# Kernel optimization log

Measured on AMD Instinct MI355X. Metric: run time of the kernel, lower is better.

Reference implementation:

```python
import jax, jax.numpy as jnp
import numpy as np

B, T, D_IN = 512, 128, 256
H1, H2 = 1024, 1024
LABEL_DIM = 3


def _lstm_layer(x, W, U, b):
    """Run one keras-LSTMCell layer over x: [T, B, D_in] -> [T, B, H].

    Keras gate order is (i, f, g, o); c' = f*c + i*tanh(g); h = o*tanh(c').
    """
    H = U.shape[0]
    batch = x.shape[1]

    def step(carry, xt):
        h, c = carry
        z = xt @ W + h @ U + b  # [B, 4H]
        i, f, g, o = jnp.split(z, 4, axis=-1)
        i = jax.nn.sigmoid(i)
        f = jax.nn.sigmoid(f)
        g = jnp.tanh(g)
        o = jax.nn.sigmoid(o)
        c_new = f * c + i * g
        h_new = o * jnp.tanh(c_new)
        return (h_new, c_new), h_new

    init = (jnp.zeros((batch, H), x.dtype), jnp.zeros((batch, H), x.dtype))
    _, hs = jax.lax.scan(step, init, x)
    return hs  # [T, B, H]


def setup_inputs() -> dict:
    key = jax.random.key(0)
    ks = jax.random.split(key, 10)
    chars = jax.random.normal(ks[0], (B, T, D_IN), dtype=jnp.float32)
    # sequence lengths in [1, T] so sequence_length - 1 is a valid index
    sequence_length = jax.random.randint(ks[1], (B,), 1, T + 1)
    s = 0.05
    W1 = jax.random.normal(ks[2], (D_IN, 4 * H1), dtype=jnp.float32) * s
    U1 = jax.random.normal(ks[3], (H1, 4 * H1), dtype=jnp.float32) * s
    b1 = jnp.zeros((4 * H1,), dtype=jnp.float32)
    W2 = jax.random.normal(ks[4], (H1, 4 * H2), dtype=jnp.float32) * s
    U2 = jax.random.normal(ks[5], (H2, 4 * H2), dtype=jnp.float32) * s
    b2 = jnp.zeros((4 * H2,), dtype=jnp.float32)
    Wd = jax.random.normal(ks[6], (H2, LABEL_DIM), dtype=jnp.float32) * s
    bd = jnp.zeros((LABEL_DIM,), dtype=jnp.float32)
    return {"chars": chars, "sequence_length": sequence_length,
            "W1": W1, "U1": U1, "b1": b1,
            "W2": W2, "U2": U2, "b2": b2,
            "Wd": Wd, "bd": bd}


def reference(chars, sequence_length, W1, U1, b1, W2, U2, b2, Wd, bd):
    # chars: [B, T, 256] -> time-major [T, B, 256]
    x = jnp.transpose(chars, (1, 0, 2))
    x = _lstm_layer(x, W1, U1, b1)          # [T, B, H1]
    x = _lstm_layer(x, W2, U2, b2)          # [T, B, H2]
    # gather the hidden state at the last valid timestep of each sequence
    batch = chars.shape[0]
    hidden = x[sequence_length - 1, jnp.arange(batch)]  # [B, H2]
    return jax.nn.relu(hidden @ Wd + bd)    # [B, label_dim]
```

## Files before the change

kernel.cpp:

```cpp
#include <hip/hip_runtime.h>
#include <hip/hip_bf16.h>


typedef __hip_bfloat16 bf16;
typedef __attribute__((ext_vector_type(8))) short bfrag8;
typedef __attribute__((ext_vector_type(4))) float accf4;

#define BATCH 512
#define TSTEPS 128
#define DIN 256
#define H 1024
#define NG 4096

__device__ __forceinline__ float sigm(float x) { return 1.0f / (1.0f + __expf(-x)); }
__device__ __forceinline__ float tanh_f(float x) {
    float a = fabsf(x);
    float e = __expf(-2.0f * a);
    float t = (1.0f - e) / (1.0f + e);
    return x < 0.0f ? -t : t;
}
__device__ __forceinline__ unsigned short bfr16(float x) {
    bf16 h = __float2bfloat16(x);
    return *(unsigned short*)&h;
}
__device__ __forceinline__ void gll16(const void* g, void* l) {
    __builtin_amdgcn_global_load_lds(
        (const __attribute__((address_space(1))) unsigned int*)g,
        (__attribute__((address_space(3))) unsigned int*)l, 16, 0, 0);
}
__device__ __forceinline__ void gll16c(const void* g, void* l) {
    __builtin_amdgcn_global_load_lds(
        (const __attribute__((address_space(1))) unsigned int*)g,
        (__attribute__((address_space(3))) unsigned int*)l, 16, 0, 16);
}
__device__ __forceinline__ void store_short_coh(void* p, unsigned short v) {
    unsigned int vv = v;
    asm volatile("global_store_short %0, %1, off sc0 sc1"
                 :: "v"(p), "v"(vv) : "memory");
}

__global__ void k_repack(const float* __restrict__ W, const float* __restrict__ U,
                         bf16* __restrict__ Bp, int KIN)
{
    __shared__ float tile[128][65];
    int kt = blockIdx.x, nt = blockIdx.y;
    int lane = threadIdx.x;
    int n = nt * 64 + lane;
    int orig = ((n >> 4) & 3) * 1024 + (n >> 7) * 32 + ((n >> 6) & 1) * 16 + (n & 15);
    for (int j = 0; j < 128; ++j) {
        int k = kt * 128 + j;
        tile[j][lane] = (k < KIN) ? W[(size_t)k * NG + orig]
                                  : U[(size_t)(k - KIN) * NG + orig];
    }
    __syncthreads();
    for (int u = 0; u < 16; ++u) {
        int cid = u * 64 + lane;
        int nloc = cid >> 4;
        int pos = cid & 15;
        int nn = nt * 64 + nloc;
        int kc = pos ^ (nn & 7);
        alignas(16) unsigned short pk[8];
        #pragma unroll
        for (int jj = 0; jj < 8; ++jj) pk[jj] = bfr16(tile[kc * 8 + jj][nloc]);
        *(int4*)(Bp + ((size_t)kt * NG + nn) * 128 + pos * 8) = *(int4*)pk;
    }
}

struct PP {
    const float* chars; const int* seqlen;
    const bf16* Bp1; const bf16* Bp2;
    const float* b1; const float* b2;
    bf16* h1; bf16* h2; float* hidden;
    int* cnt1; int* cnt2;
};

__global__ __launch_bounds__(256, 2) void k_persist(PP P)
{
    __shared__ __align__(16) bf16 Alds[64 * 128];
    __shared__ __align__(16) bf16 Blds[128 * 128];

    const int bid = blockIdx.x;
    const int job = bid >> 8;
    const int bi = bid & 255;
    const int tid = threadIdx.x;
    const int wv = tid >> 6, lane = tid & 63;
    const int ntile = bi & 31, rg = bi >> 5;
    const int b0 = rg * 64, n0 = ntile * 128;
    const int mw = (wv & 1) * 32, nw = (wv >> 1) * 64;
    const int c = lane & 15, q = lane >> 4;

    const bf16* Bp = job ? P.Bp2 : P.Bp1;
    const float* bias = job ? P.b2 : P.b1;
    const int KT = job ? 16 : 10;
    const int ksplit = job ? 1024 : 256;
    const size_t HS = (size_t)BATCH * H;

    const int hcol = ntile * 32 + (wv >> 1) * 16 + c;
    const float bi_ = bias[hcol],         bf_ = bias[H + hcol];
    const float bg_ = bias[2 * H + hcol], bo_ = bias[3 * H + hcol];
    const int seg = hcol & ~127;
    const int kc_ = (hcol & 127) >> 3;
    const int jl = hcol & 7;
    int houti[8]; int hidi[8]; int sl[8]; float cellv[8];
    #pragma unroll
    for (int u = 0; u < 8; ++u) {
        int b = b0 + mw + (u >> 2) * 16 + q * 4 + (u & 3);
        houti[u] = b * H + seg + (((kc_ ^ (b & 7))) << 3) + jl;
        hidi[u] = b * H + hcol;
        sl[u] = job ? (P.seqlen[b] - 1) : -1;
        cellv[u] = 0.f;
    }

    int* cme = (job ? P.cnt2 : P.cnt1) + rg * 16;
    int* cn1 = P.cnt1 + rg * 16;
    int* cn2 = P.cnt2 + rg * 16;

    auto stageChars = [&](int t_, int k0) {
        #pragma unroll
        for (int uu = 0; uu < 4; ++uu) {
            int u = uu * 256 + tid;
            int r = u >> 4;
            int pos = u & 15;
            int kc = pos ^ (r & 7);
            const float* src = P.chars + (size_t)(b0 + r) * (TSTEPS * DIN)
                             + (size_t)t_ * DIN + k0 + kc * 8;
            float4 va = *(const float4*)src;
            float4 vb = *(const float4*)(src + 4);
            alignas(16) unsigned short pk[8];
            pk[0] = bfr16(va.x); pk[1] = bfr16(va.y);
            pk[2] = bfr16(va.z); pk[3] = bfr16(va.w);
            pk[4] = bfr16(vb.x); pk[5] = bfr16(vb.y);
            pk[6] = bfr16(vb.z); pk[7] = bfr16(vb.w);
            *(int4*)((char*)Alds + u * 16) = *(int4*)pk;
        }
    };
    auto stageH = [&](const bf16* Asrc, int kk0) {
        #pragma unroll
        for (int cc = 0; cc < 4; ++cc) {
            int ob = wv * 4096 + cc * 1024;
            int o = ob + lane * 16;
            int r = o >> 8;
            const char* g = (const char*)Asrc + (size_t)(b0 + r) * (H * 2)
                          + kk0 * 2 + (o & 255);
            gll16c(g, (char*)Alds + ob);
        }
    };
    auto stageB = [&](int kt) {
        const char* Bg = (const char*)Bp + ((size_t)kt * NG + n0) * 256;
        #pragma unroll
        for (int cc = 0; cc < 8; ++cc) {
            int ob = wv * 8192 + cc * 1024;
            gll16(Bg + ob + lane * 16, (char*)Blds + ob);
        }
    };

    for (int t = 0; t < TSTEPS; ++t) {
        const bf16* A0 = job ? (P.h1 + (size_t)(t & 1) * HS) : nullptr;
        const bf16* A1 = (job ? P.h2 : P.h1) + (size_t)((t + 1) & 1) * HS;
        bf16* Hout = (job ? P.h2 : P.h1) + (size_t)(t & 1) * HS;

        stageB(0);
        if (!job) stageChars(t, 0);

        int n1 = job ? 32 * (t + 1) : 32 * t;
        int n2 = job ? 32 * t       : 32 * (t - 1);
        if (tid == 0) {
            while (__hip_atomic_load(cn1, __ATOMIC_RELAXED, __HIP_MEMORY_SCOPE_AGENT) < n1 ||
                   __hip_atomic_load(cn2, __ATOMIC_RELAXED, __HIP_MEMORY_SCOPE_AGENT) < n2)
                __builtin_amdgcn_s_sleep(8);
        }
        __syncthreads();
        if (job) stageH(A0, 0);

        accf4 acc[2][4];
        #pragma unroll
        for (int i = 0; i < 2; ++i)
            #pragma unroll
            for (int jz = 0; jz < 4; ++jz) acc[i][jz] = accf4{0.f, 0.f, 0.f, 0.f};

        for (int kt = 0; kt < KT; ++kt) {
            if (kt > 0) {
                int k0 = kt << 7;
                if (!job && k0 < ksplit) stageChars(t, k0);
                else if (k0 < ksplit)    stageH(A0, k0);
                else                     stageH(A1, k0 - ksplit);
                stageB(kt);
            }
            __syncthreads();
            #pragma unroll
            for (int kk = 0; kk < 128; kk += 32) {
                int kc = (kk >> 3) + q;
                int ra = mw + c;
                int pa = (kc ^ (ra & 7)) << 3;
                bfrag8 af0 = *(const bfrag8*)(Alds + ra * 128 + pa);
                bfrag8 af1 = *(const bfrag8*)(Alds + (ra + 16) * 128 + pa);
                #pragma unroll
                for (int nt = 0; nt < 4; ++nt) {
                    int nn = nw + nt * 16 + c;
                    bfrag8 bfv = *(const bfrag8*)(Blds + nn * 128 + ((kc ^ (nn & 7)) << 3));
                    acc[0][nt] = __builtin_amdgcn_mfma_f32_16x16x32_bf16(af0, bfv, acc[0][nt], 0, 0, 0);
                    acc[1][nt] = __builtin_amdgcn_mfma_f32_16x16x32_bf16(af1, bfv, acc[1][nt], 0, 0, 0);
                }
            }
            __syncthreads();
        }

        #pragma unroll
        for (int u = 0; u < 8; ++u) {
            int mt = u >> 2, reg = u & 3;
            float ig = sigm(acc[mt][0][reg] + bi_);
            float fg = sigm(acc[mt][1][reg] + bf_);
            float gv = tanh_f(acc[mt][2][reg] + bg_);
            float og = sigm(acc[mt][3][reg] + bo_);
            float cv = fg * cellv[u] + ig * gv;
            cellv[u] = cv;
            float h = og * tanh_f(cv);
            store_short_coh((unsigned short*)Hout + houti[u], bfr16(h));
            if (job && sl[u] == t) P.hidden[hidi[u]] = h;
        }

        __builtin_amdgcn_s_waitcnt(0);
        __syncthreads();
        if (tid == 0)
            __hip_atomic_fetch_add(cme, 1, __ATOMIC_RELAXED, __HIP_MEMORY_SCOPE_AGENT);
    }
}

__global__ void k_final(const float* __restrict__ hidden, const float* __restrict__ Wd,
                        const float* __restrict__ bd, float* __restrict__ out)
{
    int b = blockIdx.x;
    int l = threadIdx.x;
    float p0 = 0.f, p1 = 0.f, p2 = 0.f;
    for (int jj = l; jj < H; jj += 64) {
        float hv = hidden[(size_t)b * H + jj];
        p0 += hv * Wd[jj * 3 + 0];
        p1 += hv * Wd[jj * 3 + 1];
        p2 += hv * Wd[jj * 3 + 2];
    }
    #pragma unroll
    for (int off = 32; off > 0; off >>= 1) {
        p0 += __shfl_down(p0, off);
        p1 += __shfl_down(p1, off);
        p2 += __shfl_down(p2, off);
    }
    if (l == 0) {
        out[b * 3 + 0] = fmaxf(p0 + bd[0], 0.f);
        out[b * 3 + 1] = fmaxf(p1 + bd[1], 0.f);
        out[b * 3 + 2] = fmaxf(p2 + bd[2], 0.f);
    }
}

extern "C" void kernel_launch(void* const* d_in, const int* in_sizes, int n_in,
                              void* d_out, int out_size, void* d_ws, size_t ws_size,
                              hipStream_t stream)
{
    const float* chars = (const float*)d_in[0];
    const int* seqlen  = (const int*)d_in[1];
    const float* W1 = (const float*)d_in[2];
    const float* U1 = (const float*)d_in[3];
    const float* b1 = (const float*)d_in[4];
    const float* W2 = (const float*)d_in[5];
    const float* U2 = (const float*)d_in[6];
    const float* b2 = (const float*)d_in[7];
    const float* Wd = (const float*)d_in[8];
    const float* bd = (const float*)d_in[9];
    float* out = (float*)d_out;

    char* ws = (char*)d_ws;
    size_t off = 0;
    bf16* Bp1 = (bf16*)(ws + off); off += (size_t)10 * NG * 128 * 2;
    bf16* Bp2 = (bf16*)(ws + off); off += (size_t)16 * NG * 128 * 2;
    bf16* h1  = (bf16*)(ws + off); off += (size_t)2 * BATCH * H * 2;
    bf16* h2  = (bf16*)(ws + off); off += (size_t)2 * BATCH * H * 2;
    float* hidden = (float*)(ws + off); off += (size_t)BATCH * H * 4;
    int* cnt1 = (int*)(ws + off); off += 8 * 16 * 4;
    int* cnt2 = (int*)(ws + off); off += 8 * 16 * 4;
    if (ws_size < off) return;

    hipMemsetAsync(h1, 0, (size_t)2 * BATCH * H * 2, stream);
    hipMemsetAsync(h2, 0, (size_t)2 * BATCH * H * 2, stream);
    hipMemsetAsync(cnt1, 0, 2 * 8 * 16 * 4, stream);

    k_repack<<<dim3(10, 64), 64, 0, stream>>>(W1, U1, Bp1, 256);
    k_repack<<<dim3(16, 64), 64, 0, stream>>>(W2, U2, Bp2, 1024);

    PP P;
    P.chars = chars; P.seqlen = seqlen;
    P.Bp1 = Bp1; P.Bp2 = Bp2; P.b1 = b1; P.b2 = b2;
    P.h1 = h1; P.h2 = h2; P.hidden = hidden;
    P.cnt1 = cnt1; P.cnt2 = cnt2;

    k_persist<<<512, 256, 0, stream>>>(P);
    k_final<<<512, 64, 0, stream>>>(hidden, Wd, bd, out);
}
```

Measured before the change: 3.687 ms.

## Load weight fragments straight to registers and double-buffer activation tiles in LDS

The weight (B) operand is no longer staged through shared memory. Each wave loads its MFMA B fragments directly from global memory into registers and prefetches the next k-tile's fragments while the current one computes. The activation tile in LDS is now double-buffered, so the loop needs one barrier per k-tile instead of two. Chars loads become nontemporal and the global-to-LDS cache policy bits change. This cuts LDS traffic and barrier stalls, at the cost of more vector registers and unswizzled global fragment loads that may coalesce less well.

Measured after the change: 8.152 ms. 121% more time.

```diff
diff --git a/kernel.cpp b/kernel.cpp
--- a/kernel.cpp
+++ b/kernel.cpp
@@ -5,6 +5,7 @@
 typedef __hip_bfloat16 bf16;
 typedef __attribute__((ext_vector_type(8))) short bfrag8;
 typedef __attribute__((ext_vector_type(4))) float accf4;
+typedef __attribute__((ext_vector_type(4))) float fvec4;
 
 #define BATCH 512
 #define TSTEPS 128
@@ -23,15 +24,10 @@
     bf16 h = __float2bfloat16(x);
     return *(unsigned short*)&h;
 }
-__device__ __forceinline__ void gll16(const void* g, void* l) {
+__device__ __forceinline__ void gll16cnt(const void* g, void* l) {
     __builtin_amdgcn_global_load_lds(
         (const __attribute__((address_space(1))) unsigned int*)g,
-        (__attribute__((address_space(3))) unsigned int*)l, 16, 0, 0);
-}
-__device__ __forceinline__ void gll16c(const void* g, void* l) {
-    __builtin_amdgcn_global_load_lds(
-        (const __attribute__((address_space(1))) unsigned int*)g,
-        (__attribute__((address_space(3))) unsigned int*)l, 16, 0, 16);
+        (__attribute__((address_space(3))) unsigned int*)l, 16, 0, 18);
 }
 __device__ __forceinline__ void store_short_coh(void* p, unsigned short v) {
     unsigned int vv = v;
@@ -56,13 +52,12 @@
     for (int u = 0; u < 16; ++u) {
         int cid = u * 64 + lane;
         int nloc = cid >> 4;
-        int pos = cid & 15;
+        int kc = cid & 15;
         int nn = nt * 64 + nloc;
-        int kc = pos ^ (nn & 7);
         alignas(16) unsigned short pk[8];
         #pragma unroll
         for (int jj = 0; jj < 8; ++jj) pk[jj] = bfr16(tile[kc * 8 + jj][nloc]);
-        *(int4*)(Bp + ((size_t)kt * NG + nn) * 128 + pos * 8) = *(int4*)pk;
+        *(int4*)(Bp + ((size_t)kt * NG + nn) * 128 + kc * 8) = *(int4*)pk;
     }
 }
 
@@ -76,8 +71,7 @@
 
 __global__ __launch_bounds__(256, 2) void k_persist(PP P)
 {
-    __shared__ __align__(16) bf16 Alds[64 * 128];
-    __shared__ __align__(16) bf16 Blds[128 * 128];
+    __shared__ __align__(16) bf16 Alds[2][64 * 128];
 
     const int bid = blockIdx.x;
     const int job = bid >> 8;
@@ -89,7 +83,7 @@
     const int mw = (wv & 1) * 32, nw = (wv >> 1) * 64;
     const int c = lane & 15, q = lane >> 4;
 
-    const bf16* Bp = job ? P.Bp2 : P.Bp1;
+    const bf16* __restrict__ Bp = job ? P.Bp2 : P.Bp1;
     const float* bias = job ? P.b2 : P.b1;
     const int KT = job ? 16 : 10;
     const int ksplit = job ? 1024 : 256;
@@ -115,26 +109,35 @@
     int* cn1 = P.cnt1 + rg * 16;
     int* cn2 = P.cnt2 + rg * 16;
 
-    auto stageChars = [&](int t_, int k0) {
+    const size_t bOff = (size_t)(n0 + nw + c) * 128 + q * 8;
+    bfrag8 Bfr[4][4];
+    auto loadBg = [&](int kt, int g) {
+        const bf16* Bt = Bp + (size_t)kt * (NG * 128) + bOff + g * 32;
+        #pragma unroll
+        for (int nt = 0; nt < 4; ++nt)
+            Bfr[g][nt] = *(const bfrag8*)(Bt + nt * (16 * 128));
+    };
+
+    auto stageChars = [&](int t_, int k0, bf16* dst) {
         #pragma unroll
         for (int uu = 0; uu < 4; ++uu) {
             int u = uu * 256 + tid;
             int r = u >> 4;
             int pos = u & 15;
             int kc = pos ^ (r & 7);
-            const float* src = P.chars + (size_t)(b0 + r) * (TSTEPS * DIN)
-                             + (size_t)t_ * DIN + k0 + kc * 8;
-            float4 va = *(const float4*)src;
-            float4 vb = *(const float4*)(src + 4);
+            const fvec4* src = (const fvec4*)(P.chars
+                + (size_t)(b0 + r) * (TSTEPS * DIN) + (size_t)t_ * DIN + k0 + kc * 8);
+            fvec4 va = __builtin_nontemporal_load(src);
+            fvec4 vb = __builtin_nontemporal_load(src + 1);
             alignas(16) unsigned short pk[8];
             pk[0] = bfr16(va.x); pk[1] = bfr16(va.y);
             pk[2] = bfr16(va.z); pk[3] = bfr16(va.w);
             pk[4] = bfr16(vb.x); pk[5] = bfr16(vb.y);
             pk[6] = bfr16(vb.z); pk[7] = bfr16(vb.w);
-            *(int4*)((char*)Alds + u * 16) = *(int4*)pk;
+            *(int4*)((char*)dst + u * 16) = *(int4*)pk;
         }
     };
-    auto stageH = [&](const bf16* Asrc, int kk0) {
+    auto stageH = [&](const bf16* Asrc, int kk0, bf16* dst) {
         #pragma unroll
         for (int cc = 0; cc < 4; ++cc) {
             int ob = wv * 4096 + cc * 1024;
@@ -142,25 +145,19 @@
             int r = o >> 8;
             const char* g = (const char*)Asrc + (size_t)(b0 + r) * (H * 2)
                           + kk0 * 2 + (o & 255);
-            gll16c(g, (char*)Alds + ob);
+            gll16cnt(g, (char*)dst + ob);
         }
     };
-    auto stageB = [&](int kt) {
-        const char* Bg = (const char*)Bp + ((size_t)kt * NG + n0) * 256;
-        #pragma unroll
-        for (int cc = 0; cc < 8; ++cc) {
-            int ob = wv * 8192 + cc * 1024;
-            gll16(Bg + ob + lane * 16, (char*)Blds + ob);
-        }
-    };
+
+    #pragma unroll
+    for (int g = 0; g < 4; ++g) loadBg(0, g);
 
     for (int t = 0; t < TSTEPS; ++t) {
         const bf16* A0 = job ? (P.h1 + (size_t)(t & 1) * HS) : nullptr;
         const bf16* A1 = (job ? P.h2 : P.h1) + (size_t)((t + 1) & 1) * HS;
         bf16* Hout = (job ? P.h2 : P.h1) + (size_t)(t & 1) * HS;
 
-        stageB(0);
-        if (!job) stageChars(t, 0);
+        if (!job) stageChars(t, 0, Alds[0]);
 
         int n1 = job ? 32 * (t + 1) : 32 * t;
         int n2 = job ? 32 * t       : 32 * (t - 1);
@@ -170,7 +167,7 @@
                 __builtin_amdgcn_s_sleep(8);
         }
         __syncthreads();
-        if (job) stageH(A0, 0);
+        if (job) stageH(A0, 0, Alds[0]);
 
         accf4 acc[2][4];
         #pragma unroll
@@ -179,30 +176,29 @@
             for (int jz = 0; jz < 4; ++jz) acc[i][jz] = accf4{0.f, 0.f, 0.f, 0.f};
 
         for (int kt = 0; kt < KT; ++kt) {
-            if (kt > 0) {
-                int k0 = kt << 7;
-                if (!job && k0 < ksplit) stageChars(t, k0);
-                else if (k0 < ksplit)    stageH(A0, k0);
-                else                     stageH(A1, k0 - ksplit);
-                stageB(kt);
+            __syncthreads();
+            if (kt + 1 < KT) {
+                int k0n = (kt + 1) << 7;
+                bf16* dst = Alds[(kt + 1) & 1];
+                if (!job && k0n < ksplit)  stageChars(t, k0n, dst);
+                else if (k0n < ksplit)     stageH(A0, k0n, dst);
+                else                       stageH(A1, k0n - ksplit, dst);
             }
-            __syncthreads();
+            const bf16* Ab = Alds[kt & 1];
             #pragma unroll
-            for (int kk = 0; kk < 128; kk += 32) {
-                int kc = (kk >> 3) + q;
+            for (int g = 0; g < 4; ++g) {
+                int kc = (g << 2) + q;
                 int ra = mw + c;
                 int pa = (kc ^ (ra & 7)) << 3;
-                bfrag8 af0 = *(const bfrag8*)(Alds + ra * 128 + pa);
-                bfrag8 af1 = *(const bfrag8*)(Alds + (ra + 16) * 128 + pa);
+                bfrag8 af0 = *(const bfrag8*)(Ab + ra * 128 + pa);
+                bfrag8 af1 = *(const bfrag8*)(Ab + (ra + 16) * 128 + pa);
                 #pragma unroll
                 for (int nt = 0; nt < 4; ++nt) {
-                    int nn = nw + nt * 16 + c;
-                    bfrag8 bfv = *(const bfrag8*)(Blds + nn * 128 + ((kc ^ (nn & 7)) << 3));
-                    acc[0][nt] = __builtin_amdgcn_mfma_f32_16x16x32_bf16(af0, bfv, acc[0][nt], 0, 0, 0);
-                    acc[1][nt] = __builtin_amdgcn_mfma_f32_16x16x32_bf16(af1, bfv, acc[1][nt], 0, 0, 0);
+                    acc[0][nt] = __builtin_amdgcn_mfma_f32_16x16x32_bf16(af0, Bfr[g][nt], acc[0][nt], 0, 0, 0);
+                    acc[1][nt] = __builtin_amdgcn_mfma_f32_16x16x32_bf16(af1, Bfr[g][nt], acc[1][nt], 0, 0, 0);
                 }
+                if (kt + 1 < KT) loadBg(kt + 1, g);
             }
-            __syncthreads();
         }
 
         #pragma unroll
@@ -223,6 +219,11 @@
         __syncthreads();
         if (tid == 0)
             __hip_atomic_fetch_add(cme, 1, __ATOMIC_RELAXED, __HIP_MEMORY_SCOPE_AGENT);
+
+        if (t + 1 < TSTEPS) {
+            #pragma unroll
+            for (int g = 0; g < 4; ++g) loadBg(0, g);
+        }
     }
 }
 
@@ -278,9 +279,9 @@
     int* cnt2 = (int*)(ws + off); off += 8 * 16 * 4;
     if (ws_size < off) return;
 
-    hipMemsetAsync(h1, 0, (size_t)2 * BATCH * H * 2, stream);
-    hipMemsetAsync(h2, 0, (size_t)2 * BATCH * H * 2, stream);
-    hipMemsetAsync(cnt1, 0, 2 * 8 * 16 * 4, stream);
+    (void)hipMemsetAsync(h1, 0, (size_t)2 * BATCH * H * 2, stream);
+    (void)hipMemsetAsync(h2, 0, (size_t)2 * BATCH * H * 2, stream);
+    (void)hipMemsetAsync(cnt1, 0, 2 * 8 * 16 * 4, stream);
 
     k_repack<<<dim3(10, 64), 64, 0, stream>>>(W1, U1, Bp1, 256);
     k_repack<<<dim3(16, 64), 64, 0, stream>>>(W2, U2, Bp2, 1024);
```

## Assign persistent work tiles by XCC id so each die reuses its weight slice in L2

Applied to the files above, without the earlier changes.

Each block reads its hardware XCC id and takes a work slot from a per-XCC atomic queue, falling back to other XCCs when its own is full. The slot fixes the job, n-tile and row group, so every XCC serves a fixed set of n-tiles for both layers. The intent is that each die's L2 keeps holding the same weight columns across timesteps instead of each die pulling all columns. The change also alters the cache-policy bits on the h-state LDS loads and makes the chars loads nontemporal. It adds an atomic at block start, and correctness depends on all 512 blocks getting distinct slots.

New measurement: 4.922 ms. 1.33x slower.

```diff
diff --git a/kernel.cpp b/kernel.cpp
--- a/kernel.cpp
+++ b/kernel.cpp
@@ -5,6 +5,7 @@
 typedef __hip_bfloat16 bf16;
 typedef __attribute__((ext_vector_type(8))) short bfrag8;
 typedef __attribute__((ext_vector_type(4))) float accf4;
+typedef __attribute__((ext_vector_type(4))) float fvec4;
 
 #define BATCH 512
 #define TSTEPS 128
@@ -28,10 +29,10 @@
         (const __attribute__((address_space(1))) unsigned int*)g,
         (__attribute__((address_space(3))) unsigned int*)l, 16, 0, 0);
 }
-__device__ __forceinline__ void gll16c(const void* g, void* l) {
+__device__ __forceinline__ void gll16cnt(const void* g, void* l) {
     __builtin_amdgcn_global_load_lds(
         (const __attribute__((address_space(1))) unsigned int*)g,
-        (__attribute__((address_space(3))) unsigned int*)l, 16, 0, 16);
+        (__attribute__((address_space(3))) unsigned int*)l, 16, 0, 18);
 }
 __device__ __forceinline__ void store_short_coh(void* p, unsigned short v) {
     unsigned int vv = v;
@@ -72,24 +73,41 @@
     const float* b1; const float* b2;
     bf16* h1; bf16* h2; float* hidden;
     int* cnt1; int* cnt2;
+    int* q;
 };
 
 __global__ __launch_bounds__(256, 2) void k_persist(PP P)
 {
     __shared__ __align__(16) bf16 Alds[64 * 128];
     __shared__ __align__(16) bf16 Blds[128 * 128];
-
-    const int bid = blockIdx.x;
-    const int job = bid >> 8;
-    const int bi = bid & 255;
+    __shared__ int jobslot;
+
     const int tid = threadIdx.x;
+    if (tid == 0) {
+        unsigned int x;
+        asm volatile("s_getreg_b32 %0, hwreg(HW_REG_XCC_ID)" : "=s"(x));
+        x &= 7;
+        int got = -1;
+        for (int i = 0; i < 8 && got < 0; ++i) {
+            int y = (x + i) & 7;
+            int s = atomicAdd(P.q + y * 16, 1);
+            if (s < 64) got = (y << 6) | s;
+        }
+        jobslot = got;
+    }
+    __syncthreads();
+    const int gslot = jobslot;
+    const int y = gslot >> 6, s = gslot & 63;
+    const int job = s & 1;
+    const int ntile = y + (((s >> 1) & 3) << 3);
+    const int rg = s >> 3;
+
     const int wv = tid >> 6, lane = tid & 63;
-    const int ntile = bi & 31, rg = bi >> 5;
     const int b0 = rg * 64, n0 = ntile * 128;
     const int mw = (wv & 1) * 32, nw = (wv >> 1) * 64;
     const int c = lane & 15, q = lane >> 4;
 
-    const bf16* Bp = job ? P.Bp2 : P.Bp1;
+    const bf16* __restrict__ Bp = job ? P.Bp2 : P.Bp1;
     const float* bias = job ? P.b2 : P.b1;
     const int KT = job ? 16 : 10;
     const int ksplit = job ? 1024 : 256;
@@ -122,10 +140,10 @@
             int r = u >> 4;
             int pos = u & 15;
             int kc = pos ^ (r & 7);
-            const float* src = P.chars + (size_t)(b0 + r) * (TSTEPS * DIN)
-                             + (size_t)t_ * DIN + k0 + kc * 8;
-            float4 va = *(const float4*)src;
-            float4 vb = *(const float4*)(src + 4);
+            const fvec4* src = (const fvec4*)(P.chars
+                + (size_t)(b0 + r) * (TSTEPS * DIN) + (size_t)t_ * DIN + k0 + kc * 8);
+            fvec4 va = __builtin_nontemporal_load(src);
+            fvec4 vb = __builtin_nontemporal_load(src + 1);
             alignas(16) unsigned short pk[8];
             pk[0] = bfr16(va.x); pk[1] = bfr16(va.y);
             pk[2] = bfr16(va.z); pk[3] = bfr16(va.w);
@@ -142,7 +160,7 @@
             int r = o >> 8;
             const char* g = (const char*)Asrc + (size_t)(b0 + r) * (H * 2)
                           + kk0 * 2 + (o & 255);
-            gll16c(g, (char*)Alds + ob);
+            gll16cnt(g, (char*)Alds + ob);
         }
     };
     auto stageB = [&](int kt) {
@@ -276,11 +294,12 @@
     float* hidden = (float*)(ws + off); off += (size_t)BATCH * H * 4;
     int* cnt1 = (int*)(ws + off); off += 8 * 16 * 4;
     int* cnt2 = (int*)(ws + off); off += 8 * 16 * 4;
+    int* qq   = (int*)(ws + off); off += 8 * 16 * 4;
     if (ws_size < off) return;
 
-    hipMemsetAsync(h1, 0, (size_t)2 * BATCH * H * 2, stream);
-    hipMemsetAsync(h2, 0, (size_t)2 * BATCH * H * 2, stream);
-    hipMemsetAsync(cnt1, 0, 2 * 8 * 16 * 4, stream);
+    (void)hipMemsetAsync(h1, 0, (size_t)2 * BATCH * H * 2, stream);
+    (void)hipMemsetAsync(h2, 0, (size_t)2 * BATCH * H * 2, stream);
+    (void)hipMemsetAsync(cnt1, 0, 3 * 8 * 16 * 4, stream);
 
     k_repack<<<dim3(10, 64), 64, 0, stream>>>(W1, U1, Bp1, 256);
     k_repack<<<dim3(16, 64), 64, 0, stream>>>(W2, U2, Bp2, 1024);
@@ -289,7 +308,7 @@
     P.chars = chars; P.seqlen = seqlen;
     P.Bp1 = Bp1; P.Bp2 = Bp2; P.b1 = b1; P.b2 = b2;
     P.h1 = h1; P.h2 = h2; P.hidden = hidden;
-    P.cnt1 = cnt1; P.cnt2 = cnt2;
+    P.cnt1 = cnt1; P.cnt2 = cnt2; P.q = qq;
 
     k_persist<<<512, 256, 0, stream>>>(P);
     k_final<<<512, 64, 0, stream>>>(hidden, Wd, bd, out);
```
